# Optimization experiments

Measured on AMD Instinct MI355X. Metric: run time of the kernel, lower is better.

## Reference

```python
import jax, jax.numpy as jnp
import numpy as np

WS = 8        # window_size
SHIFT = 4     # shift_size
DS = 16       # d_state
DTR = 4       # dt_rank = ceil(hidden_dim/16)


def _win_part(x, ws):
    # (B,H,W,C) -> (B*nH*nW, ws*ws, C)
    B, H, W, C = x.shape
    x = x.reshape(B, H // ws, ws, W // ws, ws, C).transpose(0, 1, 3, 2, 4, 5)
    return x.reshape(-1, ws * ws, C)


def _win_rev(xw, ws, B, H, W):
    C = xw.shape[-1]
    x = xw.reshape(B, H // ws, W // ws, ws, ws, C).transpose(0, 1, 3, 2, 4, 5)
    return x.reshape(B, H, W, C)


def _ln(x, g, b):
    mu = x.mean(-1, keepdims=True)
    var = x.var(-1, keepdims=True)
    return (x - mu) / jnp.sqrt(var + 1e-5) * g + b


def _conv2d(v, w, b, pad):
    out = jax.lax.conv_general_dilated(v, w, (1, 1), [(pad, pad), (pad, pad)],
                                       dimension_numbers=('NCHW', 'OIHW', 'NCHW'))
    return out + b[None, :, None, None]


def setup_inputs() -> dict:
    key = jax.random.key(0)
    B, C, H, W = 2, 64, 192, 192
    di = 128  # expand * hidden_dim
    ks = jax.random.split(key, 12)

    def n(k, shape, s=0.02):
        return jax.random.normal(k, shape, jnp.float32) * s

    return {
        'x': jax.random.normal(ks[0], (B, C, H, W), jnp.float32),
        'ln1_g': jnp.ones((C,), jnp.float32), 'ln1_b': jnp.zeros((C,), jnp.float32),
        'in_w': n(ks[1], (C, 2 * di)), 'in_b': jnp.zeros((2 * di,), jnp.float32),
        'conv_w': n(ks[2], (4, di), 0.1), 'conv_b': jnp.zeros((di,), jnp.float32),
        'xproj_w': n(ks[3], (di, DTR + 2 * DS)),
        'dt_w': n(ks[4], (DTR, di), 0.1),
        'dt_b': jnp.full((di,), float(np.log(np.expm1(0.01))), jnp.float32),
        'A_log': jnp.log(jnp.tile(jnp.arange(1, DS + 1, dtype=jnp.float32), (di, 1))),
        'D': jnp.ones((di,), jnp.float32),
        'out_w': n(ks[5], (di, C)), 'out_b': jnp.zeros((C,), jnp.float32),
        'skip1': jnp.ones((C,), jnp.float32),
        'ln2_g': jnp.ones((C,), jnp.float32), 'ln2_b': jnp.zeros((C,), jnp.float32),
        'skip2': jnp.ones((C,), jnp.float32),
        'cab_w1': n(ks[6], (C // 4, C, 3, 3), 0.05), 'cab_b1': jnp.zeros((C // 4,), jnp.float32),
        'cab_w2': n(ks[7], (C, C // 4, 3, 3), 0.05), 'cab_b2': jnp.zeros((C,), jnp.float32),
        'ca_wd': n(ks[8], (C // 16, C, 1, 1), 0.05), 'ca_bd': jnp.zeros((C // 16,), jnp.float32),
        'ca_wu': n(ks[9], (C, C // 16, 1, 1), 0.05), 'ca_bu': jnp.zeros((C,), jnp.float32),
    }


def reference(x, ln1_g, ln1_b, in_w, in_b, conv_w, conv_b, xproj_w, dt_w, dt_b,
              A_log, D, out_w, out_b, skip1, ln2_g, ln2_b, skip2,
              cab_w1, cab_b1, cab_w2, cab_b2, ca_wd, ca_bd, ca_wu, ca_bu):
    B, C, H, W = x.shape
    shortcut = x.transpose(0, 2, 3, 1)  # (B,H,W,C)
    # H,W divisible by WS -> no padding, pad mask is None
    xp = jnp.roll(shortcut, (-SHIFT, -SHIFT), axis=(1, 2))
    shift_mask = jnp.zeros((B, H, W, 1), x.dtype).at[:, :H - SHIFT, :W - SHIFT, :].set(1.0)
    mask_w = _win_part(shift_mask, WS)  # (N, L, 1)

    xn = _ln(xp, ln1_g, ln1_b)
    # --- SW_HSS3D: windowed Mamba selective-scan mixer ---
    xz = xn @ in_w + in_b
    x_in, z = jnp.split(xz, 2, axis=-1)
    xw = _win_part(x_in, WS) * mask_w        # (N, L, di)
    zw = _win_part(z, WS)
    K = conv_w.shape[0]
    L = xw.shape[1]
    xpad = jnp.pad(xw, ((0, 0), (K - 1, 0), (0, 0)))  # causal depthwise conv1d
    xc = sum(xpad[:, k:k + L, :] * conv_w[k] for k in range(K)) + conv_b
    xc = jax.nn.silu(xc)
    dbc = xc @ xproj_w
    dt = jax.nn.softplus(dbc[..., :DTR] @ dt_w + dt_b)  # (N,L,di)
    Bm = dbc[..., DTR:DTR + DS]
    Cm = dbc[..., DTR + DS:]
    A = -jnp.exp(A_log)  # (di,DS)

    def step(h, t):
        dt_t, B_t, C_t, x_t = t
        h = jnp.exp(dt_t[..., None] * A) * h + (dt_t * x_t)[..., None] * B_t[:, None, :]
        y = jnp.einsum('nds,ns->nd', h, C_t)
        return h, y

    N, di = xc.shape[0], xc.shape[-1]
    h0 = jnp.zeros((N, di, DS), xc.dtype)
    xs = (dt.transpose(1, 0, 2), Bm.transpose(1, 0, 2), Cm.transpose(1, 0, 2), xc.transpose(1, 0, 2))
    _, ys = jax.lax.scan(step, h0, xs)
    y = ys.transpose(1, 0, 2) + D * xc
    y = y * jax.nn.silu(zw)
    out = y @ out_w + out_b  # (N,L,C)
    xb = _win_rev(out, WS, B, H, W)
    # NOTE: source computes roll-back but overwrites it: depad uses x_back_win directly.
    x1 = shortcut * skip1 + xb
    # --- CAB conv FFN with channel attention ---
    x2 = _ln(x1, ln2_g, ln2_b).transpose(0, 3, 1, 2)  # (B,C,H,W)
    c = _conv2d(x2, cab_w1, cab_b1, 1)
    c = jax.nn.gelu(c, approximate=False)
    c = _conv2d(c, cab_w2, cab_b2, 1)
    att = c.mean(axis=(2, 3), keepdims=True)
    att = jax.nn.relu(_conv2d(att, ca_wd, ca_bd, 0))
    att = jax.nn.sigmoid(_conv2d(att, ca_wu, ca_bu, 0))
    cab = c * att
    x_out = x1 * skip2 + cab.transpose(0, 2, 3, 1)
    return x_out.transpose(0, 3, 1, 2)
```

## Files before the change

kernel.cpp:

```cpp
#include <hip/hip_runtime.h>
#include <hip/hip_bf16.h>
#include <math.h>

#define Hh 192
#define Ww 192
#define HWp (Hh*Ww)
#define Bb 2
#define Cch 64
#define DI 128
#define NWX 24
#define WPB 576
#define NW  1152
#define DS 16
#define SHIFT 4

typedef __attribute__((ext_vector_type(8))) short short8v;
typedef __attribute__((ext_vector_type(4))) float f32x4;

__global__ __launch_bounds__(256) void k_prep(
    const float* __restrict__ in_w, const float* __restrict__ out_w,
    const float* __restrict__ w1, const float* __restrict__ w2, const float* __restrict__ xp,
    __hip_bfloat16* __restrict__ inT, __hip_bfloat16* __restrict__ outT,
    __hip_bfloat16* __restrict__ w1i, __hip_bfloat16* __restrict__ w2i,
    float* __restrict__ xpi, float* __restrict__ sums){
  int i = blockIdx.x*256 + threadIdx.x;
  if (i < 18432) {
    int o = i/72, c = i%72;
    inT[i] = (__hip_bfloat16)((c < 64) ? in_w[c*256 + o] : 0.f);
    return;
  }
  i -= 18432;
  if (i < 8704) {
    int o = i/136, c = i%136;
    outT[i] = (__hip_bfloat16)((c < 128) ? out_w[c*64 + o] : 0.f);
    return;
  }
  i -= 8704;
  if (i < 10368) {
    int tap = i/1152, r = i%1152, co = r/72, ci = r%72;
    w1i[i] = (__hip_bfloat16)((ci < 64) ? w1[(co*64 + ci)*9 + tap] : 0.f);
    return;
  }
  i -= 10368;
  if (i < 12800) {
    int p = i/2560, r = i%2560, co = r/40, k = r%40;
    float v = 0.f;
    if (k < 32) { int tap = p*2 + (k>>4); int ci = k & 15; if (tap < 9) v = w2[co*144 + ci*9 + tap]; }
    w2i[i] = (__hip_bfloat16)v;
    return;
  }
  i -= 12800;
  if (i < 4736) {
    int c = i/37, j = i%37;
    xpi[i] = (j < 36) ? xp[c*36 + j] : 0.f;
    return;
  }
  i -= 4736;
  if (i < 128) sums[i] = 0.f;
}

__global__ __launch_bounds__(256) void k_transpose(const float* __restrict__ x, __hip_bfloat16* __restrict__ xT){
  __shared__ float t[64][65];
  int b   = blockIdx.x / WPB;
  int hw0 = (blockIdx.x % WPB) * 64;
  int lane = threadIdx.x & 63, grp = threadIdx.x >> 6;
  const float* xb = x + (size_t)b * Cch * HWp;
  #pragma unroll
  for (int r = 0; r < 64; r += 4) {
    int c = r + grp;
    t[c][lane] = xb[(size_t)c * HWp + hw0 + lane];
  }
  __syncthreads();
  __hip_bfloat16* xo = xT + ((size_t)b * HWp + hw0) * 64;
  #pragma unroll
  for (int r = 0; r < 64; r += 4) {
    int hwl = r + grp;
    xo[(size_t)hwl * 64 + lane] = (__hip_bfloat16)t[lane][hwl];
  }
}

__global__ __launch_bounds__(256) void k_stage1(
    const __hip_bfloat16* __restrict__ xT, const float* __restrict__ g1, const float* __restrict__ b1,
    const __hip_bfloat16* __restrict__ inT, const float* __restrict__ in_b,
    const float* __restrict__ conv_w, const float* __restrict__ conv_b,
    const float* __restrict__ xpi,
    __hip_bfloat16* __restrict__ xc, __hip_bfloat16* __restrict__ Zb, float* __restrict__ dbc){
  __shared__ __align__(16) __hip_bfloat16 xs[64][72];
  __shared__ __align__(16) __hip_bfloat16 wt[256][72];
  __shared__ __align__(16) float XZ[64][132];
  float* wsx = reinterpret_cast<float*>(&wt[0][0]);
  int n = blockIdx.x;
  int b = n / WPB, wi = n % WPB;
  int wy = wi / NWX, wx = wi % NWX;
  int tid = threadIdx.x;
  {
    short8v* dst = reinterpret_cast<short8v*>(&wt[0][0]);
    const short8v* src = reinterpret_cast<const short8v*>(inT);
    for (int idx = tid; idx < 2304; idx += 256) dst[idx] = src[idx];
  }
  {
    int l = tid >> 2, q = tid & 3;
    int iy = l >> 3, ix = l & 7;
    int h = wy*8 + iy, w = wx*8 + ix;
    int hs = h + SHIFT; if (hs >= Hh) hs -= Hh;
    int ws2 = w + SHIFT; if (ws2 >= Ww) ws2 -= Ww;
    const __hip_bfloat16* src = xT + ((size_t)b*HWp + (size_t)hs*Ww + ws2) * 64 + q*16;
    __hip_bfloat16 tv[16];
    *reinterpret_cast<short8v*>(&tv[0]) = *reinterpret_cast<const short8v*>(src);
    *reinterpret_cast<short8v*>(&tv[8]) = *reinterpret_cast<const short8v*>(src + 8);
    float v[16];
    float s1 = 0.f, s2 = 0.f;
    #pragma unroll
    for (int i = 0; i < 16; i++) { v[i] = __bfloat162float(tv[i]); s1 += v[i]; s2 += v[i]*v[i]; }
    s1 += __shfl_xor(s1, 1); s2 += __shfl_xor(s2, 1);
    s1 += __shfl_xor(s1, 2); s2 += __shfl_xor(s2, 2);
    float mu = s1 * (1.f/64.f);
    float var = s2 * (1.f/64.f) - mu*mu;
    float rstd = rsqrtf(var + 1e-5f);
    __hip_bfloat16 tmp[16];
    #pragma unroll
    for (int i = 0; i < 16; i++) {
      int c = q*16 + i;
      tmp[i] = (__hip_bfloat16)((v[i]-mu)*rstd*g1[c] + b1[c]);
    }
    *reinterpret_cast<short8v*>(&xs[l][q*16])     = *reinterpret_cast<short8v*>(&tmp[0]);
    *reinterpret_cast<short8v*>(&xs[l][q*16 + 8]) = *reinterpret_cast<short8v*>(&tmp[8]);
  }
  __syncthreads();
  {
    int w = tid >> 6, lane = tid & 63;
    int col = lane & 15, g = lane >> 4;
    short8v af[4][2];
    #pragma unroll
    for (int m = 0; m < 4; m++)
      #pragma unroll
      for (int kh = 0; kh < 2; kh++)
        af[m][kh] = *reinterpret_cast<const short8v*>(&xs[m*16 + col][kh*32 + g*8]);
    f32x4 acc[4][4];
    #pragma unroll
    for (int m = 0; m < 4; m++)
      #pragma unroll
      for (int nt = 0; nt < 4; nt++)
        acc[m][nt] = (f32x4){0.f,0.f,0.f,0.f};
    #pragma unroll
    for (int nt = 0; nt < 4; nt++) {
      int o = (w*4 + nt)*16 + col;
      #pragma unroll
      for (int kh = 0; kh < 2; kh++) {
        short8v bf = *reinterpret_cast<const short8v*>(&wt[o][kh*32 + g*8]);
        #pragma unroll
        for (int m = 0; m < 4; m++)
          acc[m][nt] = __builtin_amdgcn_mfma_f32_16x16x32_bf16(af[m][kh], bf, acc[m][nt], 0, 0, 0);
      }
    }
    #pragma unroll
    for (int nt = 0; nt < 4; nt++) {
      int colg = (w*4 + nt)*16 + col;
      float bias = in_b[colg];
      #pragma unroll
      for (int m = 0; m < 4; m++) {
        #pragma unroll
        for (int j = 0; j < 4; j++) {
          int row = m*16 + g*4 + j;
          float val = acc[m][nt][j] + bias;
          if (colg < 128) XZ[row][colg] = val;
          else Zb[((size_t)n*64 + row)*128 + (colg - 128)] = (__hip_bfloat16)val;
        }
      }
    }
  }
  __syncthreads();
  {
    int d = tid & 127, half = tid >> 7;
    int t0 = half * 32;
    float cw0 = conv_w[d], cw1 = conv_w[128+d], cw2 = conv_w[256+d], cw3 = conv_w[384+d];
    float cb = conv_b[d];
    float p1 = 0.f, p2 = 0.f, p3 = 0.f;
    if (half) {
      int hh, ww2;
      hh = wy*8 + (31>>3); ww2 = wx*8 + (31&7);
      p1 = XZ[31][d] * ((hh < Hh-SHIFT && ww2 < Ww-SHIFT) ? 1.f : 0.f);
      hh = wy*8 + (30>>3); ww2 = wx*8 + (30&7);
      p2 = XZ[30][d] * ((hh < Hh-SHIFT && ww2 < Ww-SHIFT) ? 1.f : 0.f);
      hh = wy*8 + (29>>3); ww2 = wx*8 + (29&7);
      p3 = XZ[29][d] * ((hh < Hh-SHIFT && ww2 < Ww-SHIFT) ? 1.f : 0.f);
    }
    __syncthreads();
    __hip_bfloat16* Xn = xc + (size_t)n*8192;
    #pragma unroll 4
    for (int i = 0; i < 32; i++) {
      int t = t0 + i;
      int hh = wy*8 + (t>>3), ww2 = wx*8 + (t&7);
      float m = (hh < Hh-SHIFT && ww2 < Ww-SHIFT) ? 1.f : 0.f;
      float xv = XZ[t][d] * m;
      float pre = cw3*xv + cw2*p1 + cw1*p2 + cw0*p3 + cb;
      float sv = pre / (1.f + __expf(-pre));
      Xn[t*128 + d] = (__hip_bfloat16)sv;
      XZ[t][d] = sv;
      p3 = p2; p2 = p1; p1 = xv;
    }
  }
  __syncthreads();
  {
    float4* dst = reinterpret_cast<float4*>(wsx);
    const float4* src = reinterpret_cast<const float4*>(xpi);
    for (int idx = tid; idx < 1184; idx += 256) dst[idx] = src[idx];
  }
  __syncthreads();
  {
    int t = tid >> 2, jq = tid & 3;
    float acc[9];
    #pragma unroll
    for (int u = 0; u < 9; u++) acc[u] = 0.f;
    for (int c = 0; c < 128; c++) {
      float xv = XZ[t][c];
      #pragma unroll
      for (int u = 0; u < 9; u++) acc[u] += xv * wsx[c*37 + jq*9+u];
    }
    float* dst = dbc + ((size_t)n*64 + t)*36 + jq*9;
    #pragma unroll
    for (int u = 0; u < 9; u++) dst[u] = acc[u];
  }
}

__global__ __launch_bounds__(128) void k_scan3(
    __hip_bfloat16* __restrict__ xc,
    const __hip_bfloat16* __restrict__ Zb, const float* __restrict__ dbc,
    const float* __restrict__ dt_w, const float* __restrict__ dt_b,
    const float* __restrict__ A_log, const float* __restrict__ Dp){
  int n = blockIdx.x;
  int d = threadIdx.x;
  const float* Dn = dbc + (size_t)n*2304;
  float dtb  = dt_b[d];
  float dtw0 = dt_w[d], dtw1 = dt_w[128+d], dtw2 = dt_w[256+d], dtw3 = dt_w[384+d];
  float Dd = Dp[d];
  float a[16];
  bool pow_ok = true;
  #pragma unroll
  for (int s = 0; s < 16; s++) {
    a[s] = -__expf(A_log[d*16+s]);
    pow_ok = pow_ok && (__builtin_fabsf(a[s] + (float)(s+1)) < 1e-3f);
  }
  float h[16];
  #pragma unroll
  for (int s = 0; s < 16; s++) h[s] = 0.f;
  const __hip_bfloat16* Xn = xc + (size_t)n*8192;
  const __hip_bfloat16* Zn = Zb + (size_t)n*8192;
  __hip_bfloat16* Gn = xc + (size_t)n*8192;
  if (pow_ok) {
    #pragma unroll 2
    for (int i = 0; i < 64; i++) {
      const float* row = Dn + i*36;
      float4 dv = *reinterpret_cast<const float4*>(row);
      float4 B0 = *reinterpret_cast<const float4*>(row + 4);
      float4 B1 = *reinterpret_cast<const float4*>(row + 8);
      float4 B2 = *reinterpret_cast<const float4*>(row + 12);
      float4 B3 = *reinterpret_cast<const float4*>(row + 16);
      float4 C0 = *reinterpret_cast<const float4*>(row + 20);
      float4 C1 = *reinterpret_cast<const float4*>(row + 24);
      float4 C2 = *reinterpret_cast<const float4*>(row + 28);
      float4 C3 = *reinterpret_cast<const float4*>(row + 32);
      float pre = dtb + dv.x*dtw0 + dv.y*dtw1 + dv.z*dtw2 + dv.w*dtw3;
      float dtv = (pre > 15.f) ? pre : __logf(1.f + __expf(pre));
      float xcv = __bfloat162float(Xn[i*128 + d]);
      float zv  = __bfloat162float(Zn[i*128 + d]);
      float du  = dtv * xcv;
      float P[16];
      P[0] = __expf(-dtv);
      #pragma unroll
      for (int s = 1; s < 16; s++) {
        int aa = (s-1) >> 1, bb = (s-1) - aa;
        P[s] = P[aa] * P[bb];
      }
      h[0]  = P[0]*h[0]  + du*B0.x;  h[1]  = P[1]*h[1]  + du*B0.y;
      h[2]  = P[2]*h[2]  + du*B0.z;  h[3]  = P[3]*h[3]  + du*B0.w;
      h[4]  = P[4]*h[4]  + du*B1.x;  h[5]  = P[5]*h[5]  + du*B1.y;
      h[6]  = P[6]*h[6]  + du*B1.z;  h[7]  = P[7]*h[7]  + du*B1.w;
      h[8]  = P[8]*h[8]  + du*B2.x;  h[9]  = P[9]*h[9]  + du*B2.y;
      h[10] = P[10]*h[10]+ du*B2.z;  h[11] = P[11]*h[11]+ du*B2.w;
      h[12] = P[12]*h[12]+ du*B3.x;  h[13] = P[13]*h[13]+ du*B3.y;
      h[14] = P[14]*h[14]+ du*B3.z;  h[15] = P[15]*h[15]+ du*B3.w;
      float y0 = h[0]*C0.x + h[1]*C0.y;   y0 += h[2]*C0.z + h[3]*C0.w;
      float y1 = h[4]*C1.x + h[5]*C1.y;   y1 += h[6]*C1.z + h[7]*C1.w;
      float y2 = h[8]*C2.x + h[9]*C2.y;   y2 += h[10]*C2.z + h[11]*C2.w;
      float y3 = h[12]*C3.x + h[13]*C3.y; y3 += h[14]*C3.z + h[15]*C3.w;
      float y = (y0 + y1) + (y2 + y3);
      float yv = y + Dd*xcv;
      Gn[i*128 + d] = (__hip_bfloat16)(yv * (zv / (1.f + __expf(-zv))));
    }
  } else {
    #pragma unroll 2
    for (int i = 0; i < 64; i++) {
      const float* row = Dn + i*36;
      float4 dv = *reinterpret_cast<const float4*>(row);
      float pre = dtb + dv.x*dtw0 + dv.y*dtw1 + dv.z*dtw2 + dv.w*dtw3;
      float dtv = (pre > 15.f) ? pre : __logf(1.f + __expf(pre));
      float xcv = __bfloat162float(Xn[i*128 + d]);
      float zv  = __bfloat162float(Zn[i*128 + d]);
      float du  = dtv * xcv;
      float y = 0.f;
      #pragma unroll
      for (int s = 0; s < 16; s++) {
        float e = __expf(dtv * a[s]);
        h[s] = e*h[s] + du*row[4+s];
        y += h[s]*row[20+s];
      }
      float yv = y + Dd*xcv;
      Gn[i*128 + d] = (__hip_bfloat16)(yv * (zv / (1.f + __expf(-zv))));
    }
  }
}

__global__ __launch_bounds__(256) void k_out(
    const __hip_bfloat16* __restrict__ xT, const __hip_bfloat16* __restrict__ g,
    const __hip_bfloat16* __restrict__ outT, const float* __restrict__ out_b,
    const float* __restrict__ skip1, const float* __restrict__ g2, const float* __restrict__ b2,
    __hip_bfloat16* __restrict__ x1, __hip_bfloat16* __restrict__ x2){
  __shared__ __align__(16) __hip_bfloat16 gs[64][136];
  __shared__ __align__(16) __hip_bfloat16 wt[64][136];
  __shared__ float outs[64][65];
  int n = blockIdx.x;
  int b = n / WPB, wi = n % WPB;
  int wy = wi / NWX, wx = wi % NWX;
  int tid = threadIdx.x;
  {
    const short8v* src = reinterpret_cast<const short8v*>(g + (size_t)n*8192);
    for (int idx = tid; idx < 1024; idx += 256) {
      int t = idx >> 4, seg = idx & 15;
      *reinterpret_cast<short8v*>(&gs[t][seg*8]) = src[idx];
    }
  }
  {
    short8v* dst = reinterpret_cast<short8v*>(&wt[0][0]);
    const short8v* wsrc = reinterpret_cast<const short8v*>(outT);
    for (int idx = tid; idx < 1088; idx += 256) dst[idx] = wsrc[idx];
  }
  __syncthreads();
  {
    int w = tid >> 6, lane = tid & 63;
    int col = lane & 15, gq = lane >> 4;
    f32x4 acc[4] = {{0.f,0.f,0.f,0.f},{0.f,0.f,0.f,0.f},{0.f,0.f,0.f,0.f},{0.f,0.f,0.f,0.f}};
    #pragma unroll
    for (int kh = 0; kh < 4; kh++) {
      short8v af = *reinterpret_cast<const short8v*>(&gs[w*16 + col][kh*32 + gq*8]);
      #pragma unroll
      for (int nt = 0; nt < 4; nt++) {
        short8v bf = *reinterpret_cast<const short8v*>(&wt[nt*16 + col][kh*32 + gq*8]);
        acc[nt] = __builtin_amdgcn_mfma_f32_16x16x32_bf16(af, bf, acc[nt], 0, 0, 0);
      }
    }
    #pragma unroll
    for (int nt = 0; nt < 4; nt++) {
      int o = nt*16 + col;
      float bias = out_b[o];
      #pragma unroll
      for (int j = 0; j < 4; j++)
        outs[w*16 + gq*4 + j][o] = acc[nt][j] + bias;
    }
  }
  __syncthreads();
  int l = tid >> 2, q = tid & 3;
  int hh = wy*8 + (l>>3), ww2 = wx*8 + (l&7);
  size_t T = (size_t)b*HWp + (size_t)hh*Ww + ww2;
  __hip_bfloat16 sc[16];
  *reinterpret_cast<short8v*>(&sc[0]) = *reinterpret_cast<const short8v*>(&xT[T*64 + q*16]);
  *reinterpret_cast<short8v*>(&sc[8]) = *reinterpret_cast<const short8v*>(&xT[T*64 + q*16 + 8]);
  float v[16];
  float s1 = 0.f, s2 = 0.f;
  #pragma unroll
  for (int i = 0; i < 16; i++) {
    int c = q*16 + i;
    float val = __bfloat162float(sc[i]) * skip1[c] + outs[l][c];
    v[i] = val; s1 += val; s2 += val*val;
  }
  s1 += __shfl_xor(s1, 1); s2 += __shfl_xor(s2, 1);
  s1 += __shfl_xor(s1, 2); s2 += __shfl_xor(s2, 2);
  float mu = s1*(1.f/64.f);
  float var = s2*(1.f/64.f) - mu*mu;
  float rstd = rsqrtf(var + 1e-5f);
  __hip_bfloat16 t1[16], t2[16];
  #pragma unroll
  for (int i = 0; i < 16; i++) {
    int c = q*16 + i;
    t1[i] = (__hip_bfloat16)v[i];
    t2[i] = (__hip_bfloat16)((v[i]-mu)*rstd*g2[c] + b2[c]);
  }
  *reinterpret_cast<short8v*>(&x1[T*64 + q*16])     = *reinterpret_cast<short8v*>(&t1[0]);
  *reinterpret_cast<short8v*>(&x1[T*64 + q*16 + 8]) = *reinterpret_cast<short8v*>(&t1[8]);
  *reinterpret_cast<short8v*>(&x2[T*64 + q*16])     = *reinterpret_cast<short8v*>(&t2[0]);
  *reinterpret_cast<short8v*>(&x2[T*64 + q*16 + 8]) = *reinterpret_cast<short8v*>(&t2[8]);
}

__global__ __launch_bounds__(256) void k_conv1(
    const __hip_bfloat16* __restrict__ x2, const __hip_bfloat16* __restrict__ w1i, const float* __restrict__ bc1,
    __hip_bfloat16* __restrict__ c1){
  __shared__ __align__(16) __hip_bfloat16 xt[100][72];
  __shared__ __align__(16) __hip_bfloat16 wt[9][16][72];
  int b = blockIdx.x / WPB;
  int r = blockIdx.x % WPB;
  int by = r / NWX, bx = r % NWX;
  {
    short8v* dst = reinterpret_cast<short8v*>(&wt[0][0][0]);
    const short8v* src = reinterpret_cast<const short8v*>(w1i);
    for (int idx = threadIdx.x; idx < 1296; idx += 256) dst[idx] = src[idx];
  }
  for (int idx = threadIdx.x; idx < 800; idx += 256) {
    int p = idx >> 3, seg = idx & 7;
    int gy = by*8 + p/10 - 1;
    int gx = bx*8 + p%10 - 1;
    short8v v = {0,0,0,0,0,0,0,0};
    if (gy >= 0 && gy < Hh && gx >= 0 && gx < Ww)
      v = *reinterpret_cast<const short8v*>(&x2[((size_t)b*HWp + (size_t)gy*Ww + gx)*64 + seg*8]);
    *reinterpret_cast<short8v*>(&xt[p][seg*8]) = v;
  }
  __syncthreads();
  int wv = threadIdx.x >> 6;
  int l  = threadIdx.x & 63;
  int col = l & 15, g = l >> 4;
  int apix = wv*16 + col;
  int apy = apix >> 3, apx = apix & 7;
  f32x4 acc = {0.f,0.f,0.f,0.f};
  #pragma unroll
  for (int tap = 0; tap < 9; tap++) {
    int ky = tap/3, kx = tap%3;
    const __hip_bfloat16* arow = &xt[(apy+ky)*10 + apx+kx][0];
    #pragma unroll
    for (int kh = 0; kh < 2; kh++) {
      short8v af = *reinterpret_cast<const short8v*>(&arow[kh*32 + g*8]);
      short8v bf = *reinterpret_cast<const short8v*>(&wt[tap][col][kh*32 + g*8]);
      acc = __builtin_amdgcn_mfma_f32_16x16x32_bf16(af, bf, acc, 0, 0, 0);
    }
  }
  float bias = bc1[col];
  #pragma unroll
  for (int j = 0; j < 4; j++) {
    int opix = wv*16 + g*4 + j;
    int oy = by*8 + (opix>>3), ox = bx*8 + (opix&7);
    float v = acc[j] + bias;
    float gv = 0.5f * v * (1.f + erff(v * 0.70710678118f));
    c1[((size_t)b*HWp + (size_t)oy*Ww + ox)*16 + col] = (__hip_bfloat16)gv;
  }
}

__global__ __launch_bounds__(256) void k_conv2(
    const __hip_bfloat16* __restrict__ c1, const __hip_bfloat16* __restrict__ w2i, const float* __restrict__ bc2,
    __hip_bfloat16* __restrict__ c2, float* __restrict__ sums){
  __shared__ __align__(16) __hip_bfloat16 xt[100][16];
  __shared__ __align__(16) __hip_bfloat16 wt[5][64][40];
  __shared__ float red[4][64];
  int b = blockIdx.x / WPB;
  int r = blockIdx.x % WPB;
  int by = r / NWX, bx = r % NWX;
  {
    short8v* dst = reinterpret_cast<short8v*>(&wt[0][0][0]);
    const short8v* src = reinterpret_cast<const short8v*>(w2i);
    for (int idx = threadIdx.x; idx < 1600; idx += 256) dst[idx] = src[idx];
  }
  for (int idx = threadIdx.x; idx < 400; idx += 256) {
    int p = idx >> 2, c4 = idx & 3;
    int gy = by*8 + p/10 - 1;
    int gx = bx*8 + p%10 - 1;
    ushort4 v = {0,0,0,0};
    if (gy >= 0 && gy < Hh && gx >= 0 && gx < Ww)
      v = *reinterpret_cast<const ushort4*>(&c1[((size_t)b*HWp + (size_t)gy*Ww + gx)*16 + c4*4]);
    *reinterpret_cast<ushort4*>(&xt[p][c4*4]) = v;
  }
  __syncthreads();
  int wv4 = threadIdx.x >> 6;
  int l   = threadIdx.x & 63;
  int col = l & 15, g = l >> 4;
  int apix = wv4*16 + col;
  int apy = apix >> 3, apx = apix & 7;
  f32x4 acc[4] = {{0.f,0.f,0.f,0.f},{0.f,0.f,0.f,0.f},{0.f,0.f,0.f,0.f},{0.f,0.f,0.f,0.f}};
  #pragma unroll
  for (int p = 0; p < 5; p++) {
    int tap = p*2 + (g >> 1); if (tap > 8) tap = 8;
    int ky = tap/3, kx = tap%3;
    short8v af = *reinterpret_cast<const short8v*>(&xt[(apy+ky)*10 + apx+kx][(g&1)*8]);
    #pragma unroll
    for (int ct = 0; ct < 4; ct++) {
      short8v bf = *reinterpret_cast<const short8v*>(&wt[p][ct*16 + col][g*8]);
      acc[ct] = __builtin_amdgcn_mfma_f32_16x16x32_bf16(af, bf, acc[ct], 0, 0, 0);
    }
  }
  #pragma unroll
  for (int ct = 0; ct < 4; ct++) {
    int co = ct*16 + col;
    float bias = bc2[co];
    float part = 0.f;
    #pragma unroll
    for (int j = 0; j < 4; j++) {
      int opix = wv4*16 + g*4 + j;
      int oy = by*8 + (opix>>3), ox = bx*8 + (opix&7);
      float v = acc[ct][j] + bias;
      c2[((size_t)b*HWp + (size_t)oy*Ww + ox)*64 + co] = (__hip_bfloat16)v;
      part += v;
    }
    part += __shfl_xor(part, 16);
    part += __shfl_xor(part, 32);
    if (g == 0) red[wv4][co] = part;
  }
  __syncthreads();
  if (threadIdx.x < 64) {
    float s = red[0][threadIdx.x] + red[1][threadIdx.x] + red[2][threadIdx.x] + red[3][threadIdx.x];
    atomicAdd(&sums[b*64 + threadIdx.x], s);
  }
}

__global__ __launch_bounds__(256) void k_final(
    const __hip_bfloat16* __restrict__ x1, const __hip_bfloat16* __restrict__ c2,
    const float* __restrict__ skip2, const float* __restrict__ sums,
    const float* __restrict__ wd, const float* __restrict__ bd,
    const float* __restrict__ wu, const float* __restrict__ bu,
    float* __restrict__ out){
  __shared__ float t[64][65];
  __shared__ float hid_s[4];
  __shared__ float att_s[64];
  int b = blockIdx.x / WPB;
  int hw0 = (blockIdx.x % WPB) * 64;
  int lane = threadIdx.x & 63, grp = threadIdx.x >> 6;
  if (threadIdx.x < 4) {
    int j = threadIdx.x;
    float inv = 1.f / (float)HWp;
    float acc = bd[j];
    for (int c = 0; c < 64; c++) acc += wd[j*64+c] * (sums[b*64+c] * inv);
    hid_s[j] = fmaxf(acc, 0.f);
  }
  __syncthreads();
  if (threadIdx.x < 64) {
    int co = threadIdx.x;
    float acc = bu[co];
    #pragma unroll
    for (int j = 0; j < 4; j++) acc += wu[co*4+j] * hid_s[j];
    att_s[co] = 1.f / (1.f + __expf(-acc));
  }
  __syncthreads();
  float sk = skip2[lane], at = att_s[lane];
  #pragma unroll
  for (int r = 0; r < 64; r += 4) {
    int hwl = r + grp;
    size_t T = (size_t)b*HWp + hw0 + hwl;
    float xv = __bfloat162float(x1[T*64+lane]);
    float cv = __bfloat162float(c2[T*64+lane]);
    t[hwl][lane] = xv*sk + cv*at;
  }
  __syncthreads();
  float* ob = out + (size_t)b * Cch * HWp;
  #pragma unroll
  for (int r = 0; r < 64; r += 4) {
    int c = r + grp;
    ob[(size_t)c*HWp + hw0 + lane] = t[lane][c];
  }
}

extern "C" void kernel_launch(void* const* d_in, const int* in_sizes, int n_in,
                              void* d_out, int out_size, void* d_ws, size_t ws_size,
                              hipStream_t stream) {
  (void)in_sizes; (void)n_in; (void)out_size; (void)ws_size;
  const float* x      = (const float*)d_in[0];
  const float* ln1_g  = (const float*)d_in[1];
  const float* ln1_b  = (const float*)d_in[2];
  const float* in_w   = (const float*)d_in[3];
  const float* in_b   = (const float*)d_in[4];
  const float* conv_w = (const float*)d_in[5];
  const float* conv_b = (const float*)d_in[6];
  const float* xproj_w= (const float*)d_in[7];
  const float* dt_w   = (const float*)d_in[8];
  const float* dt_b   = (const float*)d_in[9];
  const float* A_log  = (const float*)d_in[10];
  const float* Dp     = (const float*)d_in[11];
  const float* out_w  = (const float*)d_in[12];
  const float* out_b  = (const float*)d_in[13];
  const float* skip1  = (const float*)d_in[14];
  const float* ln2_g  = (const float*)d_in[15];
  const float* ln2_b  = (const float*)d_in[16];
  const float* skip2  = (const float*)d_in[17];
  const float* cab_w1 = (const float*)d_in[18];
  const float* cab_b1 = (const float*)d_in[19];
  const float* cab_w2 = (const float*)d_in[20];
  const float* cab_b2 = (const float*)d_in[21];
  const float* ca_wd  = (const float*)d_in[22];
  const float* ca_bd  = (const float*)d_in[23];
  const float* ca_wu  = (const float*)d_in[24];
  const float* ca_bu  = (const float*)d_in[25];

  float* ws   = (float*)d_ws;
  __hip_bfloat16* xT = (__hip_bfloat16*)ws;
  __hip_bfloat16* xc = (__hip_bfloat16*)(ws + 4718592);
  __hip_bfloat16* z  = (__hip_bfloat16*)(ws + 14155776);
  float* dbc  = ws + 23592960;
  float* sums = ws + 26247168;
  __hip_bfloat16* x1 = (__hip_bfloat16*)(ws + 14155776);
  __hip_bfloat16* x2 = (__hip_bfloat16*)(ws + 18874368);
  __hip_bfloat16* c1 = (__hip_bfloat16*)(ws + 23592960);
  __hip_bfloat16* c2 = (__hip_bfloat16*)(ws + 4718592);
  __hip_bfloat16* inT  = (__hip_bfloat16*)(ws + 26247424);
  __hip_bfloat16* outT = (__hip_bfloat16*)(ws + 26256640);
  __hip_bfloat16* w1i  = (__hip_bfloat16*)(ws + 26260992);
  __hip_bfloat16* w2i  = (__hip_bfloat16*)(ws + 26266176);
  float*          xpi  = ws + 26272576;

  k_prep<<<216, 256, 0, stream>>>(in_w, out_w, cab_w1, cab_w2, xproj_w,
                                  inT, outT, w1i, w2i, xpi, sums);
  k_transpose<<<NW, 256, 0, stream>>>(x, xT);
  k_stage1<<<NW, 256, 0, stream>>>(xT, ln1_g, ln1_b, inT, in_b, conv_w, conv_b, xpi,
                                   xc, z, dbc);
  k_scan3<<<NW, 128, 0, stream>>>(xc, z, dbc, dt_w, dt_b, A_log, Dp);
  k_out<<<NW, 256, 0, stream>>>(xT, xc, outT, out_b, skip1, ln2_g, ln2_b, x1, x2);
  k_conv1<<<NW, 256, 0, stream>>>(x2, w1i, cab_b1, c1);
  k_conv2<<<NW, 256, 0, stream>>>(c1, w2i, cab_b2, c2, sums);
  k_final<<<NW, 256, 0, stream>>>(x1, c2, skip2, sums, ca_wd, ca_bd, ca_wu, ca_bu,
                                  (float*)d_out);
}
```

Baseline: 175.7 us.

## Split stage1 into GEMM kernel and conv/x-proj kernel via bf16 buffer

Splits the fused stage1 kernel into two kernels. The first does LayerNorm plus the in-projection GEMM and writes the masked x half as bf16 to a new global buffer. The second reloads that tile into a smaller bf16 shared array to run the causal conv, SiLU and x-projection. This cuts per-block shared memory, which was large because of the fp32 XZ tile, to raise occupancy. The cost is an extra launch, a global round trip of the x tile, and bf16 rounding of the pre-conv activations.

```diff
diff --git a/kernel.cpp b/kernel.cpp
--- a/kernel.cpp
+++ b/kernel.cpp
@@ -79,16 +79,12 @@
   }
 }
 
-__global__ __launch_bounds__(256) void k_stage1(
+__global__ __launch_bounds__(256) void k_stage1a(
     const __hip_bfloat16* __restrict__ xT, const float* __restrict__ g1, const float* __restrict__ b1,
     const __hip_bfloat16* __restrict__ inT, const float* __restrict__ in_b,
-    const float* __restrict__ conv_w, const float* __restrict__ conv_b,
-    const float* __restrict__ xpi,
-    __hip_bfloat16* __restrict__ xc, __hip_bfloat16* __restrict__ Zb, float* __restrict__ dbc){
+    __hip_bfloat16* __restrict__ xcp, __hip_bfloat16* __restrict__ Zb){
   __shared__ __align__(16) __hip_bfloat16 xs[64][72];
   __shared__ __align__(16) __hip_bfloat16 wt[256][72];
-  __shared__ __align__(16) float XZ[64][132];
-  float* wsx = reinterpret_cast<float*>(&wt[0][0]);
   int n = blockIdx.x;
   int b = n / WPB, wi = n % WPB;
   int wy = wi / NWX, wx = wi % NWX;
@@ -163,11 +159,35 @@
         for (int j = 0; j < 4; j++) {
           int row = m*16 + g*4 + j;
           float val = acc[m][nt][j] + bias;
-          if (colg < 128) XZ[row][colg] = val;
-          else Zb[((size_t)n*64 + row)*128 + (colg - 128)] = (__hip_bfloat16)val;
+          if (colg < 128) {
+            int hh = wy*8 + (row>>3), ww2 = wx*8 + (row&7);
+            float mk = (hh < Hh-SHIFT && ww2 < Ww-SHIFT) ? 1.f : 0.f;
+            xcp[(size_t)n*8192 + row*128 + colg] = (__hip_bfloat16)(val * mk);
+          } else {
+            Zb[((size_t)n*64 + row)*128 + (colg - 128)] = (__hip_bfloat16)val;
+          }
         }
       }
     }
+  }
+}
+
+__global__ __launch_bounds__(256) void k_stage1b(
+    const __hip_bfloat16* __restrict__ xcp,
+    const float* __restrict__ conv_w, const float* __restrict__ conv_b,
+    const float* __restrict__ xpi,
+    __hip_bfloat16* __restrict__ xc, float* __restrict__ dbc){
+  __shared__ __align__(16) __hip_bfloat16 XZt[64][128];
+  __shared__ __align__(16) float wsx[128*37];
+  int n = blockIdx.x;
+  int tid = threadIdx.x;
+  {
+    short8v* dst = reinterpret_cast<short8v*>(&XZt[0][0]);
+    const short8v* src = reinterpret_cast<const short8v*>(xcp + (size_t)n*8192);
+    for (int idx = tid; idx < 1024; idx += 256) dst[idx] = src[idx];
+    float4* wdst = reinterpret_cast<float4*>(wsx);
+    const float4* wsrc = reinterpret_cast<const float4*>(xpi);
+    for (int idx = tid; idx < 1184; idx += 256) wdst[idx] = wsrc[idx];
   }
   __syncthreads();
   {
@@ -177,34 +197,23 @@
     float cb = conv_b[d];
     float p1 = 0.f, p2 = 0.f, p3 = 0.f;
     if (half) {
-      int hh, ww2;
-      hh = wy*8 + (31>>3); ww2 = wx*8 + (31&7);
-      p1 = XZ[31][d] * ((hh < Hh-SHIFT && ww2 < Ww-SHIFT) ? 1.f : 0.f);
-      hh = wy*8 + (30>>3); ww2 = wx*8 + (30&7);
-      p2 = XZ[30][d] * ((hh < Hh-SHIFT && ww2 < Ww-SHIFT) ? 1.f : 0.f);
-      hh = wy*8 + (29>>3); ww2 = wx*8 + (29&7);
-      p3 = XZ[29][d] * ((hh < Hh-SHIFT && ww2 < Ww-SHIFT) ? 1.f : 0.f);
+      p1 = __bfloat162float(XZt[31][d]);
+      p2 = __bfloat162float(XZt[30][d]);
+      p3 = __bfloat162float(XZt[29][d]);
     }
     __syncthreads();
     __hip_bfloat16* Xn = xc + (size_t)n*8192;
     #pragma unroll 4
     for (int i = 0; i < 32; i++) {
       int t = t0 + i;
-      int hh = wy*8 + (t>>3), ww2 = wx*8 + (t&7);
-      float m = (hh < Hh-SHIFT && ww2 < Ww-SHIFT) ? 1.f : 0.f;
-      float xv = XZ[t][d] * m;
+      float xv = __bfloat162float(XZt[t][d]);
       float pre = cw3*xv + cw2*p1 + cw1*p2 + cw0*p3 + cb;
       float sv = pre / (1.f + __expf(-pre));
-      Xn[t*128 + d] = (__hip_bfloat16)sv;
-      XZ[t][d] = sv;
+      __hip_bfloat16 sb = (__hip_bfloat16)sv;
+      Xn[t*128 + d] = sb;
+      XZt[t][d] = sb;
       p3 = p2; p2 = p1; p1 = xv;
     }
-  }
-  __syncthreads();
-  {
-    float4* dst = reinterpret_cast<float4*>(wsx);
-    const float4* src = reinterpret_cast<const float4*>(xpi);
-    for (int idx = tid; idx < 1184; idx += 256) dst[idx] = src[idx];
   }
   __syncthreads();
   {
@@ -213,7 +222,7 @@
     #pragma unroll
     for (int u = 0; u < 9; u++) acc[u] = 0.f;
     for (int c = 0; c < 128; c++) {
-      float xv = XZ[t][c];
+      float xv = __bfloat162float(XZt[t][c]);
       #pragma unroll
       for (int u = 0; u < 9; u++) acc[u] += xv * wsx[c*37 + jq*9+u];
     }
@@ -585,9 +594,10 @@
   const float* ca_bu  = (const float*)d_in[25];
 
   float* ws   = (float*)d_ws;
-  __hip_bfloat16* xT = (__hip_bfloat16*)ws;
-  __hip_bfloat16* xc = (__hip_bfloat16*)(ws + 4718592);
-  __hip_bfloat16* z  = (__hip_bfloat16*)(ws + 14155776);
+  __hip_bfloat16* xT  = (__hip_bfloat16*)ws;
+  __hip_bfloat16* xc  = (__hip_bfloat16*)(ws + 4718592);
+  __hip_bfloat16* xcp = (__hip_bfloat16*)(ws + 9437184);
+  __hip_bfloat16* z   = (__hip_bfloat16*)(ws + 14155776);
   float* dbc  = ws + 23592960;
   float* sums = ws + 26247168;
   __hip_bfloat16* x1 = (__hip_bfloat16*)(ws + 14155776);
@@ -603,8 +613,8 @@
   k_prep<<<216, 256, 0, stream>>>(in_w, out_w, cab_w1, cab_w2, xproj_w,
                                   inT, outT, w1i, w2i, xpi, sums);
   k_transpose<<<NW, 256, 0, stream>>>(x, xT);
-  k_stage1<<<NW, 256, 0, stream>>>(xT, ln1_g, ln1_b, inT, in_b, conv_w, conv_b, xpi,
-                                   xc, z, dbc);
+  k_stage1a<<<NW, 256, 0, stream>>>(xT, ln1_g, ln1_b, inT, in_b, xcp, z);
+  k_stage1b<<<NW, 256, 0, stream>>>(xcp, conv_w, conv_b, xpi, xc, dbc);
   k_scan3<<<NW, 128, 0, stream>>>(xc, z, dbc, dt_w, dt_b, A_log, Dp);
   k_out<<<NW, 256, 0, stream>>>(xT, xc, outT, out_b, skip1, ln2_g, ln2_b, x1, x2);
   k_conv1<<<NW, 256, 0, stream>>>(x2, w1i, cab_b1, c1);
```

Measured after the change: 178.1 us. About the same (+1.4%).

## Fuse selective scan into stage1 kernel keeping xc and dbc in shared memory

Applied to the files above, without the earlier changes.

Merges the scan kernel into the stage1 kernel. The projected dt/B/C rows and the conv-activated xc values stay in LDS instead of being written to and reread from global memory. This removes one launch and a large global round trip. In exchange, half of each 256-thread block sits idle during the serial scan, and the scan's parallelism is tied to stage1's block shape.

```diff
diff --git a/kernel.cpp b/kernel.cpp
--- a/kernel.cpp
+++ b/kernel.cpp
@@ -79,16 +79,19 @@
   }
 }
 
-__global__ __launch_bounds__(256) void k_stage1(
+__global__ __launch_bounds__(256) void k_stage1s(
     const __hip_bfloat16* __restrict__ xT, const float* __restrict__ g1, const float* __restrict__ b1,
     const __hip_bfloat16* __restrict__ inT, const float* __restrict__ in_b,
     const float* __restrict__ conv_w, const float* __restrict__ conv_b,
     const float* __restrict__ xpi,
-    __hip_bfloat16* __restrict__ xc, __hip_bfloat16* __restrict__ Zb, float* __restrict__ dbc){
+    const float* __restrict__ dt_w, const float* __restrict__ dt_b,
+    const float* __restrict__ A_log, const float* __restrict__ Dp,
+    __hip_bfloat16* __restrict__ xc, __hip_bfloat16* __restrict__ Zb){
   __shared__ __align__(16) __hip_bfloat16 xs[64][72];
   __shared__ __align__(16) __hip_bfloat16 wt[256][72];
   __shared__ __align__(16) float XZ[64][132];
-  float* wsx = reinterpret_cast<float*>(&wt[0][0]);
+  float* wsx   = reinterpret_cast<float*>(&wt[0][0]);
+  float* dbc_s = reinterpret_cast<float*>(&xs[0][0]);
   int n = blockIdx.x;
   int b = n / WPB, wi = n % WPB;
   int wy = wi / NWX, wx = wi % NWX;
@@ -186,7 +189,6 @@
       p3 = XZ[29][d] * ((hh < Hh-SHIFT && ww2 < Ww-SHIFT) ? 1.f : 0.f);
     }
     __syncthreads();
-    __hip_bfloat16* Xn = xc + (size_t)n*8192;
     #pragma unroll 4
     for (int i = 0; i < 32; i++) {
       int t = t0 + i;
@@ -195,7 +197,6 @@
       float xv = XZ[t][d] * m;
       float pre = cw3*xv + cw2*p1 + cw1*p2 + cw0*p3 + cb;
       float sv = pre / (1.f + __expf(-pre));
-      Xn[t*128 + d] = (__hip_bfloat16)sv;
       XZ[t][d] = sv;
       p3 = p2; p2 = p1; p1 = xv;
     }
@@ -217,96 +218,88 @@
       #pragma unroll
       for (int u = 0; u < 9; u++) acc[u] += xv * wsx[c*37 + jq*9+u];
     }
-    float* dst = dbc + ((size_t)n*64 + t)*36 + jq*9;
-    #pragma unroll
-    for (int u = 0; u < 9; u++) dst[u] = acc[u];
-  }
-}
-
-__global__ __launch_bounds__(128) void k_scan3(
-    __hip_bfloat16* __restrict__ xc,
-    const __hip_bfloat16* __restrict__ Zb, const float* __restrict__ dbc,
-    const float* __restrict__ dt_w, const float* __restrict__ dt_b,
-    const float* __restrict__ A_log, const float* __restrict__ Dp){
-  int n = blockIdx.x;
-  int d = threadIdx.x;
-  const float* Dn = dbc + (size_t)n*2304;
-  float dtb  = dt_b[d];
-  float dtw0 = dt_w[d], dtw1 = dt_w[128+d], dtw2 = dt_w[256+d], dtw3 = dt_w[384+d];
-  float Dd = Dp[d];
-  float a[16];
-  bool pow_ok = true;
-  #pragma unroll
-  for (int s = 0; s < 16; s++) {
-    a[s] = -__expf(A_log[d*16+s]);
-    pow_ok = pow_ok && (__builtin_fabsf(a[s] + (float)(s+1)) < 1e-3f);
-  }
-  float h[16];
-  #pragma unroll
-  for (int s = 0; s < 16; s++) h[s] = 0.f;
-  const __hip_bfloat16* Xn = xc + (size_t)n*8192;
-  const __hip_bfloat16* Zn = Zb + (size_t)n*8192;
-  __hip_bfloat16* Gn = xc + (size_t)n*8192;
-  if (pow_ok) {
-    #pragma unroll 2
-    for (int i = 0; i < 64; i++) {
-      const float* row = Dn + i*36;
-      float4 dv = *reinterpret_cast<const float4*>(row);
-      float4 B0 = *reinterpret_cast<const float4*>(row + 4);
-      float4 B1 = *reinterpret_cast<const float4*>(row + 8);
-      float4 B2 = *reinterpret_cast<const float4*>(row + 12);
-      float4 B3 = *reinterpret_cast<const float4*>(row + 16);
-      float4 C0 = *reinterpret_cast<const float4*>(row + 20);
-      float4 C1 = *reinterpret_cast<const float4*>(row + 24);
-      float4 C2 = *reinterpret_cast<const float4*>(row + 28);
-      float4 C3 = *reinterpret_cast<const float4*>(row + 32);
-      float pre = dtb + dv.x*dtw0 + dv.y*dtw1 + dv.z*dtw2 + dv.w*dtw3;
-      float dtv = (pre > 15.f) ? pre : __logf(1.f + __expf(pre));
-      float xcv = __bfloat162float(Xn[i*128 + d]);
-      float zv  = __bfloat162float(Zn[i*128 + d]);
-      float du  = dtv * xcv;
-      float P[16];
-      P[0] = __expf(-dtv);
-      #pragma unroll
-      for (int s = 1; s < 16; s++) {
-        int aa = (s-1) >> 1, bb = (s-1) - aa;
-        P[s] = P[aa] * P[bb];
+    #pragma unroll
+    for (int u = 0; u < 9; u++) dbc_s[t*36 + jq*9 + u] = acc[u];
+  }
+  __syncthreads();
+  if (tid < 128) {
+    int d = tid;
+    float dtb  = dt_b[d];
+    float dtw0 = dt_w[d], dtw1 = dt_w[128+d], dtw2 = dt_w[256+d], dtw3 = dt_w[384+d];
+    float Dd = Dp[d];
+    float a[16];
+    bool pow_ok = true;
+    #pragma unroll
+    for (int s = 0; s < 16; s++) {
+      a[s] = -__expf(A_log[d*16+s]);
+      pow_ok = pow_ok && (__builtin_fabsf(a[s] + (float)(s+1)) < 1e-3f);
+    }
+    float h[16];
+    #pragma unroll
+    for (int s = 0; s < 16; s++) h[s] = 0.f;
+    const __hip_bfloat16* Zn = Zb + (size_t)n*8192;
+    __hip_bfloat16* Gn = xc + (size_t)n*8192;
+    if (pow_ok) {
+      #pragma unroll 2
+      for (int i = 0; i < 64; i++) {
+        const float* row = dbc_s + i*36;
+        float4 dv = *reinterpret_cast<const float4*>(row);
+        float4 B0 = *reinterpret_cast<const float4*>(row + 4);
+        float4 B1 = *reinterpret_cast<const float4*>(row + 8);
+        float4 B2 = *reinterpret_cast<const float4*>(row + 12);
+        float4 B3 = *reinterpret_cast<const float4*>(row + 16);
+        float4 C0 = *reinterpret_cast<const float4*>(row + 20);
+        float4 C1 = *reinterpret_cast<const float4*>(row + 24);
+        float4 C2 = *reinterpret_cast<const float4*>(row + 28);
+        float4 C3 = *reinterpret_cast<const float4*>(row + 32);
+        float pre = dtb + dv.x*dtw0 + dv.y*dtw1 + dv.z*dtw2 + dv.w*dtw3;
+        float dtv = (pre > 15.f) ? pre : __logf(1.f + __expf(pre));
+        float xcv = XZ[i][d];
+        float zv  = __bfloat162float(Zn[i*128 + d]);
+        float du  = dtv * xcv;
+        float P[16];
+        P[0] = __expf(-dtv);
+        #pragma unroll
+        for (int s = 1; s < 16; s++) {
+          int aa = (s-1) >> 1, bb = (s-1) - aa;
+          P[s] = P[aa] * P[bb];
+        }
+        h[0]  = P[0]*h[0]  + du*B0.x;  h[1]  = P[1]*h[1]  + du*B0.y;
+        h[2]  = P[2]*h[2]  + du*B0.z;  h[3]  = P[3]*h[3]  + du*B0.w;
+        h[4]  = P[4]*h[4]  + du*B1.x;  h[5]  = P[5]*h[5]  + du*B1.y;
+        h[6]  = P[6]*h[6]  + du*B1.z;  h[7]  = P[7]*h[7]  + du*B1.w;
+        h[8]  = P[8]*h[8]  + du*B2.x;  h[9]  = P[9]*h[9]  + du*B2.y;
+        h[10] = P[10]*h[10]+ du*B2.z;  h[11] = P[11]*h[11]+ du*B2.w;
+        h[12] = P[12]*h[12]+ du*B3.x;  h[13] = P[13]*h[13]+ du*B3.y;
+        h[14] = P[14]*h[14]+ du*B3.z;  h[15] = P[15]*h[15]+ du*B3.w;
+        float y0 = h[0]*C0.x + h[1]*C0.y;   y0 += h[2]*C0.z + h[3]*C0.w;
+        float y1 = h[4]*C1.x + h[5]*C1.y;   y1 += h[6]*C1.z + h[7]*C1.w;
+        float y2 = h[8]*C2.x + h[9]*C2.y;   y2 += h[10]*C2.z + h[11]*C2.w;
+        float y3 = h[12]*C3.x + h[13]*C3.y; y3 += h[14]*C3.z + h[15]*C3.w;
+        float y = (y0 + y1) + (y2 + y3);
+        float yv = y + Dd*xcv;
+        Gn[i*128 + d] = (__hip_bfloat16)(yv * (zv / (1.f + __expf(-zv))));
       }
-      h[0]  = P[0]*h[0]  + du*B0.x;  h[1]  = P[1]*h[1]  + du*B0.y;
-      h[2]  = P[2]*h[2]  + du*B0.z;  h[3]  = P[3]*h[3]  + du*B0.w;
-      h[4]  = P[4]*h[4]  + du*B1.x;  h[5]  = P[5]*h[5]  + du*B1.y;
-      h[6]  = P[6]*h[6]  + du*B1.z;  h[7]  = P[7]*h[7]  + du*B1.w;
-      h[8]  = P[8]*h[8]  + du*B2.x;  h[9]  = P[9]*h[9]  + du*B2.y;
-      h[10] = P[10]*h[10]+ du*B2.z;  h[11] = P[11]*h[11]+ du*B2.w;
-      h[12] = P[12]*h[12]+ du*B3.x;  h[13] = P[13]*h[13]+ du*B3.y;
-      h[14] = P[14]*h[14]+ du*B3.z;  h[15] = P[15]*h[15]+ du*B3.w;
-      float y0 = h[0]*C0.x + h[1]*C0.y;   y0 += h[2]*C0.z + h[3]*C0.w;
-      float y1 = h[4]*C1.x + h[5]*C1.y;   y1 += h[6]*C1.z + h[7]*C1.w;
-      float y2 = h[8]*C2.x + h[9]*C2.y;   y2 += h[10]*C2.z + h[11]*C2.w;
-      float y3 = h[12]*C3.x + h[13]*C3.y; y3 += h[14]*C3.z + h[15]*C3.w;
-      float y = (y0 + y1) + (y2 + y3);
-      float yv = y + Dd*xcv;
-      Gn[i*128 + d] = (__hip_bfloat16)(yv * (zv / (1.f + __expf(-zv))));
-    }
-  } else {
-    #pragma unroll 2
-    for (int i = 0; i < 64; i++) {
-      const float* row = Dn + i*36;
-      float4 dv = *reinterpret_cast<const float4*>(row);
-      float pre = dtb + dv.x*dtw0 + dv.y*dtw1 + dv.z*dtw2 + dv.w*dtw3;
-      float dtv = (pre > 15.f) ? pre : __logf(1.f + __expf(pre));
-      float xcv = __bfloat162float(Xn[i*128 + d]);
-      float zv  = __bfloat162float(Zn[i*128 + d]);
-      float du  = dtv * xcv;
-      float y = 0.f;
-      #pragma unroll
-      for (int s = 0; s < 16; s++) {
-        float e = __expf(dtv * a[s]);
-        h[s] = e*h[s] + du*row[4+s];
-        y += h[s]*row[20+s];
+    } else {
+      #pragma unroll 2
+      for (int i = 0; i < 64; i++) {
+        const float* row = dbc_s + i*36;
+        float4 dv = *reinterpret_cast<const float4*>(row);
+        float pre = dtb + dv.x*dtw0 + dv.y*dtw1 + dv.z*dtw2 + dv.w*dtw3;
+        float dtv = (pre > 15.f) ? pre : __logf(1.f + __expf(pre));
+        float xcv = XZ[i][d];
+        float zv  = __bfloat162float(Zn[i*128 + d]);
+        float du  = dtv * xcv;
+        float y = 0.f;
+        #pragma unroll
+        for (int s = 0; s < 16; s++) {
+          float e = __expf(dtv * a[s]);
+          h[s] = e*h[s] + du*row[4+s];
+          y += h[s]*row[20+s];
+        }
+        float yv = y + Dd*xcv;
+        Gn[i*128 + d] = (__hip_bfloat16)(yv * (zv / (1.f + __expf(-zv))));
       }
-      float yv = y + Dd*xcv;
-      Gn[i*128 + d] = (__hip_bfloat16)(yv * (zv / (1.f + __expf(-zv))));
     }
   }
 }
@@ -588,7 +581,6 @@
   __hip_bfloat16* xT = (__hip_bfloat16*)ws;
   __hip_bfloat16* xc = (__hip_bfloat16*)(ws + 4718592);
   __hip_bfloat16* z  = (__hip_bfloat16*)(ws + 14155776);
-  float* dbc  = ws + 23592960;
   float* sums = ws + 26247168;
   __hip_bfloat16* x1 = (__hip_bfloat16*)(ws + 14155776);
   __hip_bfloat16* x2 = (__hip_bfloat16*)(ws + 18874368);
@@ -603,9 +595,8 @@
   k_prep<<<216, 256, 0, stream>>>(in_w, out_w, cab_w1, cab_w2, xproj_w,
                                   inT, outT, w1i, w2i, xpi, sums);
   k_transpose<<<NW, 256, 0, stream>>>(x, xT);
-  k_stage1<<<NW, 256, 0, stream>>>(xT, ln1_g, ln1_b, inT, in_b, conv_w, conv_b, xpi,
-                                   xc, z, dbc);
-  k_scan3<<<NW, 128, 0, stream>>>(xc, z, dbc, dt_w, dt_b, A_log, Dp);
+  k_stage1s<<<NW, 256, 0, stream>>>(xT, ln1_g, ln1_b, inT, in_b, conv_w, conv_b, xpi,
+                                    dt_w, dt_b, A_log, Dp, xc, z);
   k_out<<<NW, 256, 0, stream>>>(xT, xc, outT, out_b, skip1, ln2_g, ln2_b, x1, x2);
   k_conv1<<<NW, 256, 0, stream>>>(x2, w1i, cab_b1, c1);
   k_conv2<<<NW, 256, 0, stream>>>(c1, w2i, cab_b2, c2, sums);
```

New measurement: 195.8 us. +11.5%, slower.
